# Kernel optimization log

Hardware: AMD Instinct MI355X
Metric: run time of the kernel (lower is better)

The kernel has to match this reference:

```python
import jax, jax.numpy as jnp
import numpy as np

N_LAYER, N_HEAD, N_EMBD, BLOCK, B, T = 8, 8, 1024, 1024, 2, 1024
LN_EPS = 1e-5


def _ln(x, w, b):
    m = jnp.mean(x, axis=-1, keepdims=True)
    v = jnp.mean(jnp.square(x - m), axis=-1, keepdims=True)
    return (x - m) * jax.lax.rsqrt(v + LN_EPS) * w + b


def setup_inputs() -> dict:
    key = jax.random.key(0)
    ks = jax.random.split(key, 8)
    L, C = N_LAYER, N_EMBD
    rn = lambda k, shape, s=0.02: jax.random.normal(k, shape, jnp.float32) * s
    return {
        "x": jax.random.normal(ks[0], (B, T, C), jnp.float32),
        "wpe": rn(ks[1], (BLOCK, C)),
        "ln1_w": jnp.ones((L, C), jnp.float32),
        "ln1_b": jnp.zeros((L, C), jnp.float32),
        "attn_w": rn(ks[2], (L, 3 * C, C)),
        "attn_b": jnp.zeros((L, 3 * C), jnp.float32),
        "proj_w": rn(ks[3], (L, C, C), 0.02 / np.sqrt(2 * L)),
        "proj_b": jnp.zeros((L, C), jnp.float32),
        "ln2_w": jnp.ones((L, C), jnp.float32),
        "ln2_b": jnp.zeros((L, C), jnp.float32),
        "fc_w": rn(ks[4], (L, 4 * C, C)),
        "fc_b": jnp.zeros((L, 4 * C), jnp.float32),
        "fcp_w": rn(ks[5], (L, C, 4 * C), 0.02 / np.sqrt(2 * L)),
        "fcp_b": jnp.zeros((L, C), jnp.float32),
        "lnf_w": jnp.ones((C,), jnp.float32),
        "lnf_b": jnp.zeros((C,), jnp.float32),
    }


def reference(x, wpe, ln1_w, ln1_b, attn_w, attn_b, proj_w, proj_b,
              ln2_w, ln2_b, fc_w, fc_b, fcp_w, fcp_b, lnf_w, lnf_b):
    Bb, Tt, C = x.shape
    H = N_HEAD
    D = C // H
    scale = jnp.float32(1.0 / np.sqrt(D))
    h = x + wpe[:Tt][None]  # pos emb broadcast over batch; dropout = identity (eval)
    causal = jnp.tril(jnp.ones((Tt, Tt), bool))  # [T,T]

    def block(h, p):
        l1w, l1b, aw, ab, pw, pb, l2w, l2b, fw, fb, pw2, pb2 = p
        xn = _ln(h, l1w, l1b)
        qkv = xn @ aw.T + ab  # [B,T,3C]
        q, k, v = jnp.split(qkv, 3, axis=-1)
        q = q.reshape(Bb, Tt, H, D).transpose(0, 2, 1, 3)  # bhtd
        k = k.reshape(Bb, Tt, H, D).transpose(0, 2, 1, 3)
        v = v.reshape(Bb, Tt, H, D).transpose(0, 2, 1, 3)
        att = jnp.einsum('bhtd,bhsd->bhts', q, k) * scale
        att = jnp.where(causal, att, -jnp.inf)
        att = jax.nn.softmax(att, axis=-1)
        y = jnp.einsum('bhts,bhsd->bhtd', att, v)
        y = y.transpose(0, 2, 1, 3).reshape(Bb, Tt, C)
        h = h + (y @ pw.T + pb)
        xn2 = _ln(h, l2w, l2b)
        m = jax.nn.gelu(xn2 @ fw.T + fb, approximate=True)  # matches NewGELU tanh form
        h = h + (m @ pw2.T + pb2)
        return h, None

    h, _ = jax.lax.scan(block, h, (ln1_w, ln1_b, attn_w, attn_b, proj_w, proj_b,
                                   ln2_w, ln2_b, fc_w, fc_b, fcp_w, fcp_b))
    return _ln(h, lnf_w, lnf_b)
```

## Files before the change

### kernel.cpp

```cpp
#include <hip/hip_runtime.h>

typedef unsigned short u16;
typedef __attribute__((ext_vector_type(8))) short short8;
typedef __attribute__((ext_vector_type(4))) float floatx4;

__device__ __forceinline__ u16 f2b(float f){
  unsigned u = __builtin_bit_cast(unsigned, f);
  u += 0x7FFFu + ((u >> 16) & 1u);
  return (u16)(u >> 16);
}

__device__ __forceinline__ float gelu_f(float x){
  float u = 0.7978845608028654f * (x + 0.044715f * x * x * x);
  float e = __expf(2.0f * u);
  return 0.5f * x * (2.0f - 2.0f / (e + 1.0f));
}

typedef const __attribute__((address_space(1))) unsigned int gas_u32;
typedef __attribute__((address_space(3))) unsigned int las_u32;
__device__ __forceinline__ void gll16(const void* g, void* l){
  __builtin_amdgcn_global_load_lds((gas_u32*)g, (las_u32*)l, 16, 0, 0);
}

__global__ __launch_bounds__(256) void k_cvt(const float* __restrict__ src,
                                             u16* __restrict__ dst){
  size_t e = ((size_t)blockIdx.x * 256 + threadIdx.x) * 4;
  float4 v = *(const float4*)(src + e);
  ushort4 o; o.x = f2b(v.x); o.y = f2b(v.y); o.z = f2b(v.z); o.w = f2b(v.w);
  *(ushort4*)(dst + e) = o;
}

__global__ __launch_bounds__(256) void k_addpos(const float* __restrict__ x,
                                                const float* __restrict__ wpe,
                                                float* __restrict__ h){
  size_t e = ((size_t)blockIdx.x * 256 + threadIdx.x) * 4;
  float4 a = *(const float4*)(x + e);
  float4 p = *(const float4*)(wpe + (e & 1048575u));
  float4 o; o.x = a.x + p.x; o.y = a.y + p.y; o.z = a.z + p.z; o.w = a.w + p.w;
  *(float4*)(h + e) = o;
}

__global__ __launch_bounds__(256) void k_layernorm(const float* __restrict__ x,
                                                   const float* __restrict__ w,
                                                   const float* __restrict__ b,
                                                   void* __restrict__ out, int out_bf16){
  int row = blockIdx.x, t = threadIdx.x;
  const float* xr = x + (size_t)row * 1024;
  float4 v = ((const float4*)xr)[t];
  float s1 = v.x + v.y + v.z + v.w;
  float s2 = v.x*v.x + v.y*v.y + v.z*v.z + v.w*v.w;
  #pragma unroll
  for (int off = 32; off > 0; off >>= 1){
    s1 += __shfl_down(s1, off);
    s2 += __shfl_down(s2, off);
  }
  __shared__ float p1[4], p2[4];
  if ((t & 63) == 0){ p1[t >> 6] = s1; p2[t >> 6] = s2; }
  __syncthreads();
  float S1 = p1[0] + p1[1] + p1[2] + p1[3];
  float S2 = p2[0] + p2[1] + p2[2] + p2[3];
  float mean = S1 * (1.0f / 1024.0f);
  float var  = S2 * (1.0f / 1024.0f) - mean * mean;
  float rs = rsqrtf(var + 1e-5f);
  float4 wv = ((const float4*)w)[t];
  float4 bv = ((const float4*)b)[t];
  float o0 = (v.x - mean) * rs * wv.x + bv.x;
  float o1 = (v.y - mean) * rs * wv.y + bv.y;
  float o2 = (v.z - mean) * rs * wv.z + bv.z;
  float o3 = (v.w - mean) * rs * wv.w + bv.w;
  if (out_bf16){
    ushort4 o; o.x = f2b(o0); o.y = f2b(o1); o.z = f2b(o2); o.w = f2b(o3);
    ((ushort4*)((u16*)out + (size_t)row * 1024))[t] = o;
  } else {
    float4 o; o.x = o0; o.y = o1; o.z = o2; o.w = o3;
    ((float4*)((float*)out + (size_t)row * 1024))[t] = o;
  }
}

template<int MODE>
__global__ __launch_bounds__(256) void k_gemm(
    const u16* __restrict__ A, int lda,
    const u16* __restrict__ B, int ldb,
    const float* __restrict__ bias,
    void* __restrict__ Out, int ldo,
    int Kdim, int n_ntiles, int Ksplit)
{
  int bx = blockIdx.x, by = blockIdx.y;
  int nt = bx % n_ntiles, sp = bx / n_ntiles;
  int m0 = by * 128, n0 = nt * 128;
  int ks = sp * Ksplit;
  int ke = ks + Ksplit < Kdim ? ks + Ksplit : Kdim;
  if (ks >= ke) return;

  __shared__ u16 As[128 * 32];
  __shared__ u16 Bs[128 * 32];
  int t = threadIdx.x;
  int lane = t & 63, wid = t >> 6;
  int wm = (wid >> 1) * 64, wn = (wid & 1) * 64;
  int quad = lane >> 4, tm = lane & 15;
  int ar = t >> 2, ac = (t & 3) * 8;
  const u16* Ab = A + (size_t)(m0 + ar) * lda + ac;
  const u16* Bb = B + (size_t)(n0 + ar) * ldb + ac;
  u16* AsP0 = &As[t * 8];           u16* AsP1 = &As[2048 + t * 8];
  u16* BsP0 = &Bs[t * 8];           u16* BsP1 = &Bs[2048 + t * 8];
  const size_t a64 = (size_t)64 * lda, b64 = (size_t)64 * ldb;

  floatx4 acc[4][4] = {};
  for (int k0 = ks; k0 < ke; k0 += 32){
    __syncthreads();
    gll16(Ab + k0,        AsP0);
    gll16(Ab + a64 + k0,  AsP1);
    gll16(Bb + k0,        BsP0);
    gll16(Bb + b64 + k0,  BsP1);
    __syncthreads();
    short8 af[4], bf[4];
    #pragma unroll
    for (int i = 0; i < 4; i++)
      af[i] = *(const short8*)&As[(wm + i * 16 + tm) * 32 + quad * 8];
    #pragma unroll
    for (int j = 0; j < 4; j++)
      bf[j] = *(const short8*)&Bs[(wn + j * 16 + tm) * 32 + quad * 8];
    #pragma unroll
    for (int i = 0; i < 4; i++)
      #pragma unroll
      for (int j = 0; j < 4; j++)
        acc[i][j] = __builtin_amdgcn_mfma_f32_16x16x32_bf16(af[i], bf[j], acc[i][j], 0, 0, 0);
  }
  #pragma unroll
  for (int j = 0; j < 4; j++){
    int col = n0 + wn + j * 16 + tm;
    float bc = 0.0f;
    if ((MODE == 0 || MODE == 1) && bias) bc = bias[col];
    if (MODE == 2 && sp == 0 && bias) bc = bias[col];
    #pragma unroll
    for (int i = 0; i < 4; i++){
      int row0 = m0 + wm + i * 16 + quad * 4;
      #pragma unroll
      for (int r = 0; r < 4; r++){
        float v = acc[i][j][r] + bc;
        size_t idx = (size_t)(row0 + r) * ldo + col;
        if (MODE == 0)      ((u16*)Out)[idx] = f2b(v);
        else if (MODE == 1) ((u16*)Out)[idx] = f2b(gelu_f(v));
        else                atomicAdd((float*)Out + idx, v);
      }
    }
  }
}

__global__ __launch_bounds__(256) void k_transpose_v(const u16* __restrict__ vsrc,
                                                     u16* __restrict__ vt){
  __shared__ u16 tile[64][66];
  int bh = blockIdx.z, b = bh >> 3, hh = bh & 7;
  int d0 = blockIdx.x * 64, s0 = blockIdx.y * 64;
  const u16* src = vsrc + (size_t)b * 3145728 + hh * 128;
  int t = threadIdx.x;
  {
    int sr = t >> 4, c4 = (t & 15) * 4;
    #pragma unroll
    for (int p = 0; p < 4; p++){
      int s = sr + p * 16;
      ushort4 v = *(const ushort4*)(src + (size_t)(s0 + s) * 3072 + d0 + c4);
      tile[s][c4 + 0] = v.x; tile[s][c4 + 1] = v.y;
      tile[s][c4 + 2] = v.z; tile[s][c4 + 3] = v.w;
    }
  }
  __syncthreads();
  {
    int dr = t >> 4, s4 = (t & 15) * 4;
    #pragma unroll
    for (int p = 0; p < 4; p++){
      int d = dr + p * 16;
      ushort4 o;
      o.x = tile[s4 + 0][d]; o.y = tile[s4 + 1][d];
      o.z = tile[s4 + 2][d]; o.w = tile[s4 + 3][d];
      *(ushort4*)(vt + (size_t)bh * 131072 + (size_t)(d0 + d) * 1024 + s0 + s4) = o;
    }
  }
}

__global__ __launch_bounds__(256) void k_flash(const u16* __restrict__ qkv,
                                               const u16* __restrict__ vt,
                                               u16* __restrict__ yb){
  int qi = blockIdx.x, bh = blockIdx.y;
  int b = bh >> 3, hh = bh & 7;
  int t = threadIdx.x, lane = t & 63, w = t >> 6;
  int quad = lane >> 4, tm = lane & 15;
  const int q0 = qi * 64;
  const u16* Qg  = qkv + (size_t)b * 3145728 + hh * 128;
  const u16* Kg  = Qg + 1024;
  const u16* Vtg = vt + (size_t)bh * 131072;
  __shared__ u16 Ks[64 * 128];
  __shared__ u16 Vs[128 * 64];
  __shared__ u16 Ps[4][16 * 64];

  short8 qf[4];
  {
    const u16* qr = Qg + (size_t)(q0 + w * 16 + tm) * 3072 + quad * 8;
    #pragma unroll
    for (int kk = 0; kk < 4; kk++) qf[kk] = *(const short8*)(qr + kk * 32);
  }
  floatx4 o_acc[8] = {};
  float m_r[4], l_r[4];
  #pragma unroll
  for (int r = 0; r < 4; r++){ m_r[r] = -3.0e38f; l_r[r] = 0.0f; }
  const float scale = 0.08838834764831845f;

  for (int s0 = 0; s0 <= q0; s0 += 64){
    __syncthreads();
    {
      int idx = w * 256 + lane;
      #pragma unroll
      for (int p = 0; p < 4; p++){
        int id = idx + p * 64;
        gll16(Kg + (size_t)(s0 + (id >> 4)) * 3072 + (id & 15) * 8, &Ks[id * 8]);
      }
      #pragma unroll
      for (int p = 0; p < 4; p++){
        int id = idx + p * 64;
        gll16(Vtg + (size_t)(id >> 3) * 1024 + s0 + (id & 7) * 8, &Vs[id * 8]);
      }
    }
    __syncthreads();
    floatx4 s_acc[4] = {};
    #pragma unroll
    for (int j = 0; j < 4; j++)
      #pragma unroll
      for (int kk = 0; kk < 4; kk++){
        short8 kf = *(const short8*)&Ks[(j * 16 + tm) * 128 + kk * 32 + quad * 8];
        s_acc[j] = __builtin_amdgcn_mfma_f32_16x16x32_bf16(qf[kk], kf, s_acc[j], 0, 0, 0);
      }
    bool diag = (s0 == q0);
    float sv[4][4];
    #pragma unroll
    for (int j = 0; j < 4; j++)
      #pragma unroll
      for (int r = 0; r < 4; r++){
        float v = s_acc[j][r] * scale;
        if (diag && (j * 16 + tm > w * 16 + quad * 4 + r)) v = -3.0e38f;
        sv[j][r] = v;
      }
    float pv[4][4];
    #pragma unroll
    for (int r = 0; r < 4; r++){
      float m = fmaxf(fmaxf(sv[0][r], sv[1][r]), fmaxf(sv[2][r], sv[3][r]));
      #pragma unroll
      for (int off = 8; off > 0; off >>= 1) m = fmaxf(m, __shfl_xor(m, off));
      float m_new = fmaxf(m_r[r], m);
      float alpha = __expf(m_r[r] - m_new);
      m_r[r] = m_new;
      float s = 0.0f;
      #pragma unroll
      for (int j = 0; j < 4; j++){
        float p = __expf(sv[j][r] - m_new);
        pv[j][r] = p; s += p;
      }
      #pragma unroll
      for (int off = 8; off > 0; off >>= 1) s += __shfl_xor(s, off);
      l_r[r] = l_r[r] * alpha + s;
      #pragma unroll
      for (int jd = 0; jd < 8; jd++) o_acc[jd][r] *= alpha;
    }
    u16* Pw = Ps[w];
    #pragma unroll
    for (int j = 0; j < 4; j++)
      #pragma unroll
      for (int r = 0; r < 4; r++)
        Pw[(quad * 4 + r) * 64 + j * 16 + tm] = f2b(pv[j][r]);
    __syncthreads();
    short8 pf[2];
    #pragma unroll
    for (int kk = 0; kk < 2; kk++)
      pf[kk] = *(const short8*)&Pw[tm * 64 + kk * 32 + quad * 8];
    #pragma unroll
    for (int jd = 0; jd < 8; jd++)
      #pragma unroll
      for (int kk = 0; kk < 2; kk++){
        short8 vf = *(const short8*)&Vs[(jd * 16 + tm) * 64 + kk * 32 + quad * 8];
        o_acc[jd] = __builtin_amdgcn_mfma_f32_16x16x32_bf16(pf[kk], vf, o_acc[jd], 0, 0, 0);
      }
  }
  u16* yr = yb + ((size_t)b * 1024 + q0 + w * 16 + quad * 4) * 1024 + hh * 128;
  #pragma unroll
  for (int r = 0; r < 4; r++){
    float inv = 1.0f / l_r[r];
    #pragma unroll
    for (int jd = 0; jd < 8; jd++)
      yr[(size_t)r * 1024 + jd * 16 + tm] = f2b(o_acc[jd][r] * inv);
  }
}

extern "C" void kernel_launch(void* const* d_in, const int* in_sizes, int n_in,
                              void* d_out, int out_size, void* d_ws, size_t ws_size,
                              hipStream_t stream){
  const float* x     = (const float*)d_in[0];
  const float* wpe   = (const float*)d_in[1];
  const float* ln1w  = (const float*)d_in[2];
  const float* ln1b  = (const float*)d_in[3];
  const float* attnw = (const float*)d_in[4];
  const float* attnb = (const float*)d_in[5];
  const float* projw = (const float*)d_in[6];
  const float* projb = (const float*)d_in[7];
  const float* ln2w  = (const float*)d_in[8];
  const float* ln2b  = (const float*)d_in[9];
  const float* fcw   = (const float*)d_in[10];
  const float* fcb   = (const float*)d_in[11];
  const float* fcpw  = (const float*)d_in[12];
  const float* fcpb  = (const float*)d_in[13];
  const float* lnfw  = (const float*)d_in[14];
  const float* lnfb  = (const float*)d_in[15];

  char* ws = (char*)d_ws;
  float* h    = (float*)(ws);
  u16*   xn   = (u16*)(ws + 8388608);
  u16*   qkv  = (u16*)(ws + 12582912);
  u16*   vt   = (u16*)(ws + 25165824);
  u16*   yb   = (u16*)(ws + 29360128);
  u16*   mlp  = (u16*)(ws + 33554432);
  u16*   wqkv = (u16*)(ws + 50331648);
  u16*   wprj = (u16*)(ws + 100663296);
  u16*   wfc  = (u16*)(ws + 117440512);
  u16*   wfcp = (u16*)(ws + 184549376);

  k_cvt<<<24576, 256, 0, stream>>>(attnw, wqkv);
  k_cvt<<<8192,  256, 0, stream>>>(projw, wprj);
  k_cvt<<<32768, 256, 0, stream>>>(fcw,  wfc);
  k_cvt<<<32768, 256, 0, stream>>>(fcpw, wfcp);
  k_addpos<<<2048, 256, 0, stream>>>(x, wpe, h);

  for (int l = 0; l < 8; l++){
    k_layernorm<<<2048, 256, 0, stream>>>(h, ln1w + l * 1024, ln1b + l * 1024, xn, 1);
    k_gemm<0><<<dim3(24, 16), 256, 0, stream>>>(
        xn, 1024, wqkv + (size_t)l * 3145728, 1024, attnb + l * 3072,
        qkv, 3072, 1024, 24, 1024);
    k_transpose_v<<<dim3(2, 16, 16), 256, 0, stream>>>(qkv + 2048, vt);
    k_flash<<<dim3(16, 16), 256, 0, stream>>>(qkv, vt, yb);
    k_gemm<2><<<dim3(32, 16), 256, 0, stream>>>(
        yb, 1024, wprj + (size_t)l * 1048576, 1024, projb + l * 1024,
        h, 1024, 1024, 8, 256);
    k_layernorm<<<2048, 256, 0, stream>>>(h, ln2w + l * 1024, ln2b + l * 1024, xn, 1);
    k_gemm<1><<<dim3(32, 16), 256, 0, stream>>>(
        xn, 1024, wfc + (size_t)l * 4194304, 1024, fcb + l * 4096,
        mlp, 4096, 1024, 32, 1024);
    k_gemm<2><<<dim3(32, 16), 256, 0, stream>>>(
        mlp, 4096, wfcp + (size_t)l * 4194304, 4096, fcpb + l * 1024,
        h, 1024, 4096, 8, 1024);
  }
  k_layernorm<<<2048, 256, 0, stream>>>(h, lnfw, lnfb, (float*)d_out, 0);
  (void)in_sizes; (void)n_in; (void)out_size; (void)ws_size;
}
```

Baseline: 2.136 ms.

## Double-buffer GEMM and flash tiles, fuse V transpose into QKV GEMM epilogue

The GEMM and flash-attention loops now use two LDS buffers and prefetch the next K tile with global_load_lds while the current one is computed. This drops one barrier per iteration and overlaps memory with MFMA work. A new GEMM mode writes the V part of the QKV output directly in transposed layout, which removes the separate transpose kernel and its extra memory pass. In flash, the barrier before reading P is replaced by a per-wave lgkmcnt wait, and shared memory use doubles, which may lower occupancy.

```diff
diff --git a/kernel.cpp b/kernel.cpp
--- a/kernel.cpp
+++ b/kernel.cpp
@@ -83,7 +83,8 @@
     const u16* __restrict__ B, int ldb,
     const float* __restrict__ bias,
     void* __restrict__ Out, int ldo,
-    int Kdim, int n_ntiles, int Ksplit)
+    int Kdim, int n_ntiles, int Ksplit,
+    u16* __restrict__ Out2)
 {
   int bx = blockIdx.x, by = blockIdx.y;
   int nt = bx % n_ntiles, sp = bx / n_ntiles;
@@ -92,8 +93,8 @@
   int ke = ks + Ksplit < Kdim ? ks + Ksplit : Kdim;
   if (ks >= ke) return;
 
-  __shared__ u16 As[128 * 32];
-  __shared__ u16 Bs[128 * 32];
+  __shared__ u16 As[2][128 * 32];
+  __shared__ u16 Bs[2][128 * 32];
   int t = threadIdx.x;
   int lane = t & 63, wid = t >> 6;
   int wm = (wid >> 1) * 64, wn = (wid & 1) * 64;
@@ -101,79 +102,78 @@
   int ar = t >> 2, ac = (t & 3) * 8;
   const u16* Ab = A + (size_t)(m0 + ar) * lda + ac;
   const u16* Bb = B + (size_t)(n0 + ar) * ldb + ac;
-  u16* AsP0 = &As[t * 8];           u16* AsP1 = &As[2048 + t * 8];
-  u16* BsP0 = &Bs[t * 8];           u16* BsP1 = &Bs[2048 + t * 8];
   const size_t a64 = (size_t)64 * lda, b64 = (size_t)64 * ldb;
 
   floatx4 acc[4][4] = {};
+  gll16(Ab + ks,       &As[0][t * 8]);
+  gll16(Ab + a64 + ks, &As[0][2048 + t * 8]);
+  gll16(Bb + ks,       &Bs[0][t * 8]);
+  gll16(Bb + b64 + ks, &Bs[0][2048 + t * 8]);
+  __syncthreads();
+
+  int cur = 0;
   for (int k0 = ks; k0 < ke; k0 += 32){
-    __syncthreads();
-    gll16(Ab + k0,        AsP0);
-    gll16(Ab + a64 + k0,  AsP1);
-    gll16(Bb + k0,        BsP0);
-    gll16(Bb + b64 + k0,  BsP1);
-    __syncthreads();
+    int k1 = k0 + 32;
+    if (k1 < ke){
+      gll16(Ab + k1,       &As[cur ^ 1][t * 8]);
+      gll16(Ab + a64 + k1, &As[cur ^ 1][2048 + t * 8]);
+      gll16(Bb + k1,       &Bs[cur ^ 1][t * 8]);
+      gll16(Bb + b64 + k1, &Bs[cur ^ 1][2048 + t * 8]);
+    }
     short8 af[4], bf[4];
     #pragma unroll
     for (int i = 0; i < 4; i++)
-      af[i] = *(const short8*)&As[(wm + i * 16 + tm) * 32 + quad * 8];
+      af[i] = *(const short8*)&As[cur][(wm + i * 16 + tm) * 32 + quad * 8];
     #pragma unroll
     for (int j = 0; j < 4; j++)
-      bf[j] = *(const short8*)&Bs[(wn + j * 16 + tm) * 32 + quad * 8];
+      bf[j] = *(const short8*)&Bs[cur][(wn + j * 16 + tm) * 32 + quad * 8];
     #pragma unroll
     for (int i = 0; i < 4; i++)
       #pragma unroll
       for (int j = 0; j < 4; j++)
         acc[i][j] = __builtin_amdgcn_mfma_f32_16x16x32_bf16(af[i], bf[j], acc[i][j], 0, 0, 0);
-  }
-  #pragma unroll
-  for (int j = 0; j < 4; j++){
-    int col = n0 + wn + j * 16 + tm;
-    float bc = 0.0f;
-    if ((MODE == 0 || MODE == 1) && bias) bc = bias[col];
-    if (MODE == 2 && sp == 0 && bias) bc = bias[col];
-    #pragma unroll
-    for (int i = 0; i < 4; i++){
-      int row0 = m0 + wm + i * 16 + quad * 4;
-      #pragma unroll
-      for (int r = 0; r < 4; r++){
-        float v = acc[i][j][r] + bc;
-        size_t idx = (size_t)(row0 + r) * ldo + col;
-        if (MODE == 0)      ((u16*)Out)[idx] = f2b(v);
-        else if (MODE == 1) ((u16*)Out)[idx] = f2b(gelu_f(v));
-        else                atomicAdd((float*)Out + idx, v);
-      }
-    }
-  }
-}
-
-__global__ __launch_bounds__(256) void k_transpose_v(const u16* __restrict__ vsrc,
-                                                     u16* __restrict__ vt){
-  __shared__ u16 tile[64][66];
-  int bh = blockIdx.z, b = bh >> 3, hh = bh & 7;
-  int d0 = blockIdx.x * 64, s0 = blockIdx.y * 64;
-  const u16* src = vsrc + (size_t)b * 3145728 + hh * 128;
-  int t = threadIdx.x;
-  {
-    int sr = t >> 4, c4 = (t & 15) * 4;
-    #pragma unroll
-    for (int p = 0; p < 4; p++){
-      int s = sr + p * 16;
-      ushort4 v = *(const ushort4*)(src + (size_t)(s0 + s) * 3072 + d0 + c4);
-      tile[s][c4 + 0] = v.x; tile[s][c4 + 1] = v.y;
-      tile[s][c4 + 2] = v.z; tile[s][c4 + 3] = v.w;
-    }
-  }
-  __syncthreads();
-  {
-    int dr = t >> 4, s4 = (t & 15) * 4;
-    #pragma unroll
-    for (int p = 0; p < 4; p++){
-      int d = dr + p * 16;
-      ushort4 o;
-      o.x = tile[s4 + 0][d]; o.y = tile[s4 + 1][d];
-      o.z = tile[s4 + 2][d]; o.w = tile[s4 + 3][d];
-      *(ushort4*)(vt + (size_t)bh * 131072 + (size_t)(d0 + d) * 1024 + s0 + s4) = o;
+    __syncthreads();
+    cur ^= 1;
+  }
+
+  if (MODE == 3 && n0 >= 2048){
+    #pragma unroll
+    for (int j = 0; j < 4; j++){
+      int col = n0 + wn + j * 16 + tm;
+      float bc = bias ? bias[col] : 0.0f;
+      int dg = col - 2048;
+      int hh = dg >> 7, d = dg & 127;
+      #pragma unroll
+      for (int i = 0; i < 4; i++){
+        int row0 = m0 + wm + i * 16 + quad * 4;
+        int b = row0 >> 10, s = row0 & 1023;
+        ushort4 o;
+        o.x = f2b(acc[i][j][0] + bc);
+        o.y = f2b(acc[i][j][1] + bc);
+        o.z = f2b(acc[i][j][2] + bc);
+        o.w = f2b(acc[i][j][3] + bc);
+        *(ushort4*)(Out2 + (size_t)(b * 8 + hh) * 131072 + (size_t)d * 1024 + s) = o;
+      }
+    }
+  } else {
+    #pragma unroll
+    for (int j = 0; j < 4; j++){
+      int col = n0 + wn + j * 16 + tm;
+      float bc = 0.0f;
+      if ((MODE == 0 || MODE == 1 || MODE == 3) && bias) bc = bias[col];
+      if (MODE == 2 && sp == 0 && bias) bc = bias[col];
+      #pragma unroll
+      for (int i = 0; i < 4; i++){
+        int row0 = m0 + wm + i * 16 + quad * 4;
+        #pragma unroll
+        for (int r = 0; r < 4; r++){
+          float v = acc[i][j][r] + bc;
+          size_t idx = (size_t)(row0 + r) * ldo + col;
+          if (MODE == 0 || MODE == 3) ((u16*)Out)[idx] = f2b(v);
+          else if (MODE == 1)         ((u16*)Out)[idx] = f2b(gelu_f(v));
+          else                        atomicAdd((float*)Out + idx, v);
+        }
+      }
     }
   }
 }
@@ -189,9 +189,23 @@
   const u16* Qg  = qkv + (size_t)b * 3145728 + hh * 128;
   const u16* Kg  = Qg + 1024;
   const u16* Vtg = vt + (size_t)bh * 131072;
-  __shared__ u16 Ks[64 * 128];
-  __shared__ u16 Vs[128 * 64];
+  __shared__ u16 Ks[2][64 * 128];
+  __shared__ u16 Vs[2][128 * 64];
   __shared__ u16 Ps[4][16 * 64];
+
+  auto stage = [&](int s0s, int bufi){
+    int idx = w * 256 + lane;
+    #pragma unroll
+    for (int p = 0; p < 4; p++){
+      int id = idx + p * 64;
+      gll16(Kg + (size_t)(s0s + (id >> 4)) * 3072 + (id & 15) * 8, &Ks[bufi][id * 8]);
+    }
+    #pragma unroll
+    for (int p = 0; p < 4; p++){
+      int id = idx + p * 64;
+      gll16(Vtg + (size_t)(id >> 3) * 1024 + s0s + (id & 7) * 8, &Vs[bufi][id * 8]);
+    }
+  };
 
   short8 qf[4];
   {
@@ -205,28 +219,17 @@
   for (int r = 0; r < 4; r++){ m_r[r] = -3.0e38f; l_r[r] = 0.0f; }
   const float scale = 0.08838834764831845f;
 
+  stage(0, 0);
+  __syncthreads();
+  int cur = 0;
   for (int s0 = 0; s0 <= q0; s0 += 64){
-    __syncthreads();
-    {
-      int idx = w * 256 + lane;
-      #pragma unroll
-      for (int p = 0; p < 4; p++){
-        int id = idx + p * 64;
-        gll16(Kg + (size_t)(s0 + (id >> 4)) * 3072 + (id & 15) * 8, &Ks[id * 8]);
-      }
-      #pragma unroll
-      for (int p = 0; p < 4; p++){
-        int id = idx + p * 64;
-        gll16(Vtg + (size_t)(id >> 3) * 1024 + s0 + (id & 7) * 8, &Vs[id * 8]);
-      }
-    }
-    __syncthreads();
+    if (s0 + 64 <= q0) stage(s0 + 64, cur ^ 1);
     floatx4 s_acc[4] = {};
     #pragma unroll
     for (int j = 0; j < 4; j++)
       #pragma unroll
       for (int kk = 0; kk < 4; kk++){
-        short8 kf = *(const short8*)&Ks[(j * 16 + tm) * 128 + kk * 32 + quad * 8];
+        short8 kf = *(const short8*)&Ks[cur][(j * 16 + tm) * 128 + kk * 32 + quad * 8];
         s_acc[j] = __builtin_amdgcn_mfma_f32_16x16x32_bf16(qf[kk], kf, s_acc[j], 0, 0, 0);
       }
     bool diag = (s0 == q0);
@@ -266,7 +269,7 @@
       #pragma unroll
       for (int r = 0; r < 4; r++)
         Pw[(quad * 4 + r) * 64 + j * 16 + tm] = f2b(pv[j][r]);
-    __syncthreads();
+    asm volatile("s_waitcnt lgkmcnt(0)" ::: "memory");
     short8 pf[2];
     #pragma unroll
     for (int kk = 0; kk < 2; kk++)
@@ -275,9 +278,11 @@
     for (int jd = 0; jd < 8; jd++)
       #pragma unroll
       for (int kk = 0; kk < 2; kk++){
-        short8 vf = *(const short8*)&Vs[(jd * 16 + tm) * 64 + kk * 32 + quad * 8];
+        short8 vf = *(const short8*)&Vs[cur][(jd * 16 + tm) * 64 + kk * 32 + quad * 8];
         o_acc[jd] = __builtin_amdgcn_mfma_f32_16x16x32_bf16(pf[kk], vf, o_acc[jd], 0, 0, 0);
       }
+    __syncthreads();
+    cur ^= 1;
   }
   u16* yr = yb + ((size_t)b * 1024 + q0 + w * 16 + quad * 4) * 1024 + hh * 128;
   #pragma unroll
@@ -329,21 +334,20 @@
 
   for (int l = 0; l < 8; l++){
     k_layernorm<<<2048, 256, 0, stream>>>(h, ln1w + l * 1024, ln1b + l * 1024, xn, 1);
-    k_gemm<0><<<dim3(24, 16), 256, 0, stream>>>(
+    k_gemm<3><<<dim3(24, 16), 256, 0, stream>>>(
         xn, 1024, wqkv + (size_t)l * 3145728, 1024, attnb + l * 3072,
-        qkv, 3072, 1024, 24, 1024);
-    k_transpose_v<<<dim3(2, 16, 16), 256, 0, stream>>>(qkv + 2048, vt);
+        qkv, 3072, 1024, 24, 1024, vt);
     k_flash<<<dim3(16, 16), 256, 0, stream>>>(qkv, vt, yb);
     k_gemm<2><<<dim3(32, 16), 256, 0, stream>>>(
         yb, 1024, wprj + (size_t)l * 1048576, 1024, projb + l * 1024,
-        h, 1024, 1024, 8, 256);
+        h, 1024, 1024, 8, 256, (u16*)nullptr);
     k_layernorm<<<2048, 256, 0, stream>>>(h, ln2w + l * 1024, ln2b + l * 1024, xn, 1);
     k_gemm<1><<<dim3(32, 16), 256, 0, stream>>>(
         xn, 1024, wfc + (size_t)l * 4194304, 1024, fcb + l * 4096,
-        mlp, 4096, 1024, 32, 1024);
+        mlp, 4096, 1024, 32, 1024, (u16*)nullptr);
     k_gemm<2><<<dim3(32, 16), 256, 0, stream>>>(
         mlp, 4096, wfcp + (size_t)l * 4194304, 4096, fcpb + l * 1024,
-        h, 1024, 4096, 8, 1024);
+        h, 1024, 4096, 8, 1024, (u16*)nullptr);
   }
   k_layernorm<<<2048, 256, 0, stream>>>(h, lnfw, lnfb, (float*)d_out, 0);
   (void)in_sizes; (void)n_in; (void)out_size; (void)ws_size;
```

After: 2.058 ms. -3.7%, faster.
